# Kernel tuning notes

Measured on AMD Instinct MI355X. Metric: run time of the kernel, lower is better.

## Reference

```python
import jax, jax.numpy as jnp
import numpy as np

NV = 6890          # SMPL vertex count
NF = 13776         # SMPL face count
N_CHUNKS = 10
EUCL_THRES = 0.02  # euclthres
WN_THRES = 0.99    # exterior if winding number <= 0.99


def _winding_numbers(points, tris):
    """Generalized winding numbers of `points` [m,3] w.r.t. triangle soup `tris` [f,3,3].
    Solid angle per (point, triangle) via the van-Oosterom/Strackee atan2 formula."""
    r = tris[None, :, :, :] - points[:, None, None, :]   # [m,f,3,3]
    ra, rb, rc = r[:, :, 0, :], r[:, :, 1, :], r[:, :, 2, :]
    la = jnp.linalg.norm(ra, axis=-1)
    lb = jnp.linalg.norm(rb, axis=-1)
    lc = jnp.linalg.norm(rc, axis=-1)
    det = jnp.einsum('mfi,mfi->mf', ra, jnp.cross(rb, rc))
    denom = (la * lb * lc
             + jnp.sum(ra * rb, -1) * lc
             + jnp.sum(rb * rc, -1) * la
             + jnp.sum(rc * ra, -1) * lb)
    omega = 2.0 * jnp.arctan2(det, denom)                # [m,f]
    return jnp.sum(omega, axis=-1) / (4.0 * jnp.pi)      # [m]


def setup_inputs() -> dict:
    key = jax.random.key(0)
    k1, k2, k3 = jax.random.split(key, 3)
    vertices = jax.random.normal(k1, (1, NV, 3), dtype=jnp.float32)
    faces = jax.random.randint(k2, (NF, 3), 0, NV)
    # geodesic-distance >= geothres mask: symmetric, False on the diagonal
    gm = jax.random.uniform(k3, (NV, NV)) > 0.3
    gm = gm & gm.T
    gm = gm.at[jnp.arange(NV), jnp.arange(NV)].set(False)
    return {"vertices": vertices, "faces": faces, "geomask": gm}


def reference(vertices, faces, geomask):
    # triangles(vertices): gather face corner coordinates  [NF,3,3] (bs=1)
    tris = vertices[0][faces]
    # get_intersection_mask: chunked winding numbers, exterior = wn <= 0.99
    pts = vertices[0].reshape(N_CHUNKS, NV // N_CHUNKS, 3)
    wn = jax.lax.map(lambda p: _winding_numbers(p, tris), pts).reshape(NV)
    exterior = (wn <= WN_THRES)[None, :]                 # [1,NV] bool
    # batch_pairwise_dist (squared=False)
    x = vertices[0]                                      # [NV,3]
    sq = jnp.sum(x * x, axis=-1)
    d2 = sq[:, None] + sq[None, :] - 2.0 * (x @ x.T)
    v2v = jnp.sqrt(jnp.maximum(d2, 0.0))                 # [NV,NV]
    # mask geodesically-near pairs with inf, take per-vertex min over dim 1
    masked = jnp.where(geomask, v2v, jnp.inf)
    idx = jnp.argmin(masked, axis=0)                     # argmin over rows for each column
    v2v_min = v2v[jnp.arange(NV), idx][None, :]          # gather along dim 2 (symmetric)
    incontact = v2v_min < EUCL_THRES
    return v2v_min, incontact, exterior
```

## Files before the change

### kernel.cpp

```cpp
#include <hip/hip_runtime.h>
#include <math.h>

#define NV 6890
#define NF 13776
#define NVPAD 6912
#define NFPAD 13824
#define HALF 3456
#define PBLK 14
#define TCH 64
#define TPC 216
#define WN_BLOCKS (PBLK*TCH)
#define V2V_BLOCKS 1723
#define RED_BLOCKS 27
#define WN_THRES 0.99
#define EUCL_THRES 0.02f

#define WS_TRIS_OFF   64
#define WS_X4_OFF     (64 + NFPAD*48)
#define WS_PART_OFF   (WS_X4_OFF + NVPAD*16)

__global__ __launch_bounds__(256) void prep_kernel(
    const float* __restrict__ verts, const int* __restrict__ faces,
    const unsigned char* __restrict__ gm_bytes,
    float* __restrict__ tris12, float* __restrict__ x4, int* __restrict__ flag)
{
    int t = blockIdx.x * 256 + threadIdx.x;

    if (t < NFPAD) {
        float* o = tris12 + (size_t)t * 12;
        if (t < NF) {
            int ia = faces[t*3+0], ib = faces[t*3+1], ic = faces[t*3+2];
            o[0]  = verts[ia*3+0]; o[1]  = verts[ia*3+1]; o[2]  = verts[ia*3+2]; o[3]  = 0.f;
            o[4]  = verts[ib*3+0]; o[5]  = verts[ib*3+1]; o[6]  = verts[ib*3+2]; o[7]  = 0.f;
            o[8]  = verts[ic*3+0]; o[9]  = verts[ic*3+1]; o[10] = verts[ic*3+2]; o[11] = 0.f;
        } else {
            #pragma unroll
            for (int q = 0; q < 12; ++q) o[q] = 0.f;
        }
    }
    if (t < NVPAD) {
        if (t < NV) {
            float x = verts[t*3+0], y = verts[t*3+1], z = verts[t*3+2];
            x4[t*4+0] = x; x4[t*4+1] = y; x4[t*4+2] = z;
            x4[t*4+3] = (x*x + y*y) + z*z;
        } else {
            x4[t*4+0] = 0.f; x4[t*4+1] = 0.f; x4[t*4+2] = 0.f; x4[t*4+3] = 0.f;
        }
    }
    if (blockIdx.x == 0 && threadIdx.x < 64) {
        int lane = threadIdx.x;
        bool any3F = false, anyNZmod = false;
        for (int k = 0; k < 64; ++k) {
            int off = lane * 64 + k;
            unsigned char b = gm_bytes[off];
            if ((off & 3) == 3 && (b == 0x3F || b == 0xBF)) any3F = true;
            if ((off & 3) != 0 && b != 0) anyNZmod = true;
        }
        unsigned long long m3F = __ballot(any3F);
        unsigned long long mNZ = __ballot(anyNZmod);
        if (lane == 0) {
            *flag = m3F ? 2 : (mNZ ? 0 : 1);
        }
    }
}

__device__ __forceinline__ float fast_atan2f(float y, float x)
{
    float ay = __builtin_fabsf(y), ax = __builtin_fabsf(x);
    float mx = fmaxf(ax, ay);
    float mn = fminf(ax, ay);
    float r  = __builtin_amdgcn_rcpf(fmaxf(mx, 1e-37f));
    float t  = mn * r;
    float s  = t * t;
    float u  =              0.00282363896258175373077393f;
    u = fmaf(u, s, -0.0159569028764963150024414f);
    u = fmaf(u, s,  0.0425049886107444763183594f);
    u = fmaf(u, s, -0.0748900920152664184570312f);
    u = fmaf(u, s,  0.106347933411598205566406f);
    u = fmaf(u, s, -0.142027363181114196777344f);
    u = fmaf(u, s,  0.199926957488059997558594f);
    u = fmaf(u, s, -0.333331018686294555664062f);
    float p = fmaf(s * u, t, t);
    p = (ay > ax)  ? (1.5707963267948966f - p) : p;
    p = (x < 0.0f) ? (3.14159265358979323846f - p) : p;
    return copysignf(p, y);
}

#define TRI_OMEGA(A, B, C, PX, PY, PZ, S)                                 \
    {                                                                     \
        float ax = A.x - PX, ay = A.y - PY, az = A.z - PZ;                \
        float bx = B.x - PX, by = B.y - PY, bz = B.z - PZ;                \
        float cx = C.x - PX, cy = C.y - PY, cz = C.z - PZ;                \
        float la = __builtin_amdgcn_sqrtf((ax*ax + ay*ay) + az*az);       \
        float lb = __builtin_amdgcn_sqrtf((bx*bx + by*by) + bz*bz);       \
        float lc = __builtin_amdgcn_sqrtf((cx*cx + cy*cy) + cz*cz);       \
        float ux = by*cz - bz*cy;                                         \
        float uy = bz*cx - bx*cz;                                         \
        float uz = bx*cy - by*cx;                                         \
        float det = (ax*ux + ay*uy) + az*uz;                              \
        float dab = (ax*bx + ay*by) + az*bz;                              \
        float dbc = (bx*cx + by*cy) + bz*cz;                              \
        float dca = (cx*ax + cy*ay) + cz*az;                              \
        float denom = la*lb*lc + dab*lc + dbc*la + dca*lb;                \
        S += fast_atan2f(det, denom);                                     \
    }

__global__ __launch_bounds__(256) void fused_kernel(
    const float4* __restrict__ tris12, const float4* __restrict__ x4,
    float* __restrict__ partials,
    const void* __restrict__ gm, const int* __restrict__ flag_p,
    float* __restrict__ out)
{
    if (blockIdx.x < WN_BLOCKS) {
        int tc = blockIdx.x / PBLK;
        int pb = blockIdx.x - tc * PBLK;
        int pt = pb * 256 + threadIdx.x;
        if (pt >= HALF) return;
        int p1i = pt + HALF;

        float4 P0 = x4[pt];
        float4 P1 = x4[p1i];
        float px0 = P0.x, py0 = P0.y, pz0 = P0.z;
        float px1 = P1.x, py1 = P1.y, pz1 = P1.z;

        const float4* __restrict__ T = tris12 + (size_t)tc * (TPC * 3);

        float4 A0 = T[0], B0 = T[1], C0 = T[2];
        float4 A1 = T[3], B1 = T[4], C1 = T[5];
        double acc0 = 0.0, acc1 = 0.0;

        for (int kk = 0; kk < TPC; kk += 2) {
            int n0 = 3 * min(kk + 2, TPC - 1);
            int n1 = 3 * min(kk + 3, TPC - 1);
            float s0 = 0.f, s1 = 0.f;

            TRI_OMEGA(A0, B0, C0, px0, py0, pz0, s0);
            TRI_OMEGA(A0, B0, C0, px1, py1, pz1, s1);
            A0 = T[n0]; B0 = T[n0 + 1]; C0 = T[n0 + 2];

            TRI_OMEGA(A1, B1, C1, px0, py0, pz0, s0);
            TRI_OMEGA(A1, B1, C1, px1, py1, pz1, s1);
            A1 = T[n1]; B1 = T[n1 + 1]; C1 = T[n1 + 2];

            acc0 += (double)s0;
            acc1 += (double)s1;
        }

        partials[(size_t)tc * NVPAD + pt]  = (float)acc0;
        partials[(size_t)tc * NVPAD + p1i] = (float)acc1;
    } else {
        int bid = blockIdx.x - WN_BLOCKS;
        int w = threadIdx.x >> 6;
        int lane = threadIdx.x & 63;
        int j = bid * 4 + w;
        if (j >= NV) return;

        int flag = *flag_p;
        float4 vj = x4[j];
        float m = INFINITY;

#define V2V_BODY(GTEST)                                            \
        {                                                          \
            int i0 = 0;                                            \
            for (; i0 + 64 <= NV; i0 += 64) {                      \
                int i = i0 + lane;                                 \
                bool g = (GTEST);                                  \
                float4 vi = x4[i];                                 \
                float dot = (vi.x*vj.x + vi.y*vj.y) + vi.z*vj.z;   \
                float d2  = vi.w + vj.w - 2.0f*dot;                \
                m = fminf(m, g ? d2 : INFINITY);                   \
            }                                                      \
            int i = i0 + lane;                                     \
            if (i < NV) {                                          \
                bool g = (GTEST);                                  \
                float4 vi = x4[i];                                 \
                float dot = (vi.x*vj.x + vi.y*vj.y) + vi.z*vj.z;   \
                float d2  = vi.w + vj.w - 2.0f*dot;                \
                m = fminf(m, g ? d2 : INFINITY);                   \
            }                                                      \
        }

        if (flag == 0) {
            const unsigned char* row = (const unsigned char*)gm + (size_t)j * NV;
            V2V_BODY(row[i] != 0)
        } else if (flag == 1) {
            const int* row = (const int*)gm + (size_t)j * NV;
            V2V_BODY(row[i] != 0)
        } else {
            const float* row = (const float*)gm + (size_t)j * NV;
            V2V_BODY(row[i] != 0.0f)
        }
#undef V2V_BODY

        #pragma unroll
        for (int k = 32; k > 0; k >>= 1)
            m = fminf(m, __shfl_xor(m, k, 64));
        if (lane == 0) {
            float d = __builtin_amdgcn_sqrtf(fmaxf(m, 0.f));
            out[j] = d;
            out[NV + j] = (d < EUCL_THRES) ? 1.f : 0.f;
        }
    }
}

__global__ __launch_bounds__(256) void wn_reduce_kernel(
    const float* __restrict__ partials, float* __restrict__ out_exterior)
{
    int pt = blockIdx.x * 256 + threadIdx.x;
    if (pt >= NV) return;
    double s = 0.0;
    for (int t = 0; t < TCH; ++t) s += (double)partials[(size_t)t * NVPAD + pt];
    double wn = (2.0 * s) / 12.566370614359172953850573533118;
    out_exterior[pt] = (wn <= WN_THRES) ? 1.0f : 0.0f;
}

extern "C" void kernel_launch(void* const* d_in, const int* in_sizes, int n_in,
                              void* d_out, int out_size, void* d_ws, size_t ws_size,
                              hipStream_t stream)
{
    const float* verts = (const float*)d_in[0];
    const int*   faces = (const int*)d_in[1];
    const void*  gm    = d_in[2];
    float* out = (float*)d_out;
    char* ws = (char*)d_ws;

    int*   flag     = (int*)ws;
    float* tris12   = (float*)(ws + WS_TRIS_OFF);
    float* x4       = (float*)(ws + WS_X4_OFF);
    float* partials = (float*)(ws + WS_PART_OFF);

    prep_kernel<<<NFPAD / 256, 256, 0, stream>>>(
        verts, faces, (const unsigned char*)gm, tris12, x4, flag);

    fused_kernel<<<WN_BLOCKS + V2V_BLOCKS, 256, 0, stream>>>(
        (const float4*)tris12, (const float4*)x4, partials, gm, flag, out);

    wn_reduce_kernel<<<RED_BLOCKS, 256, 0, stream>>>(partials, out + 2 * NV);
}
```

Measured before the change: 441.4 us.

## Precompute all-pairs vertex distance table and reuse it for winding numbers and v2v

Adds a kernel that builds a dense NV×NVPAD table of vertex-to-vertex distances. The winding-number kernel then reads the corner distances from it and derives the dot products from per-face edge lengths, a normal and a plane offset computed in prep, so the per-pair sqrt and cross-product work goes away. The v2v min pass reads distances from the table instead of recomputing them. This trades ALU work for about 190MB of table writes and gathered reads whose row indices depend on the face, and it falls back to the old path when the workspace is too small.

```diff
diff --git a/kernel.cpp b/kernel.cpp
--- a/kernel.cpp
+++ b/kernel.cpp
@@ -6,33 +6,61 @@
 #define NVPAD 6912
 #define NFPAD 13824
 #define HALF 3456
-#define PBLK 14
-#define TCH 64
-#define TPC 216
-#define WN_BLOCKS (PBLK*TCH)
 #define V2V_BLOCKS 1723
 #define RED_BLOCKS 27
 #define WN_THRES 0.99
 #define EUCL_THRES 0.02f
 
+#define TCH_FB 64
+#define TPC_FB 216
+#define PBLK_FB 14
+#define WNB_FB (TCH_FB*PBLK_FB)
+#define TCH_TB 128
+#define TPC_TB 108
+#define PBLK_TB 14
+#define WNB_TB (TCH_TB*PBLK_TB)
+
 #define WS_TRIS_OFF   64
 #define WS_X4_OFF     (64 + NFPAD*48)
 #define WS_PART_OFF   (WS_X4_OFF + NVPAD*16)
+#define WS_TAB_OFF    (((WS_PART_OFF + TCH_TB*NVPAD*4) + 255) & ~(size_t)255)
+#define WS_TAB_BYTES  ((size_t)NV * NVPAD * 4)
 
 __global__ __launch_bounds__(256) void prep_kernel(
     const float* __restrict__ verts, const int* __restrict__ faces,
     const unsigned char* __restrict__ gm_bytes,
-    float* __restrict__ tris12, float* __restrict__ x4, int* __restrict__ flag)
+    float* __restrict__ tris, float* __restrict__ x4, int* __restrict__ flag,
+    int mode)
 {
     int t = blockIdx.x * 256 + threadIdx.x;
 
     if (t < NFPAD) {
-        float* o = tris12 + (size_t)t * 12;
+        float* o = tris + (size_t)t * 12;
         if (t < NF) {
             int ia = faces[t*3+0], ib = faces[t*3+1], ic = faces[t*3+2];
-            o[0]  = verts[ia*3+0]; o[1]  = verts[ia*3+1]; o[2]  = verts[ia*3+2]; o[3]  = 0.f;
-            o[4]  = verts[ib*3+0]; o[5]  = verts[ib*3+1]; o[6]  = verts[ib*3+2]; o[7]  = 0.f;
-            o[8]  = verts[ic*3+0]; o[9]  = verts[ic*3+1]; o[10] = verts[ic*3+2]; o[11] = 0.f;
+            float Ax = verts[ia*3+0], Ay = verts[ia*3+1], Az = verts[ia*3+2];
+            float Bx = verts[ib*3+0], By = verts[ib*3+1], Bz = verts[ib*3+2];
+            float Cx = verts[ic*3+0], Cy = verts[ic*3+1], Cz = verts[ic*3+2];
+            if (mode == 0) {
+                o[0]=Ax; o[1]=Ay; o[2]=Az;  o[3]=0.f;
+                o[4]=Bx; o[5]=By; o[6]=Bz;  o[7]=0.f;
+                o[8]=Cx; o[9]=Cy; o[10]=Cz; o[11]=0.f;
+            } else {
+                float e1x=Bx-Ax, e1y=By-Ay, e1z=Bz-Az;
+                float e2x=Cx-Ax, e2y=Cy-Ay, e2z=Cz-Az;
+                float nx = e1y*e2z - e1z*e2y;
+                float ny = e1z*e2x - e1x*e2z;
+                float nz = e1x*e2y - e1y*e2x;
+                float d0 = (nx*Ax + ny*Ay) + nz*Az;
+                float eab = (e1x*e1x + e1y*e1y) + e1z*e1z;
+                float bcx=Cx-Bx, bcy=Cy-By, bcz=Cz-Bz;
+                float ebc = (bcx*bcx + bcy*bcy) + bcz*bcz;
+                float eca = (e2x*e2x + e2y*e2y) + e2z*e2z;
+                o[0]=nx; o[1]=ny; o[2]=nz; o[3]=d0;
+                o[4]=eab; o[5]=ebc; o[6]=eca; o[7]=0.f;
+                o[8]=__int_as_float(ia); o[9]=__int_as_float(ib);
+                o[10]=__int_as_float(ic); o[11]=0.f;
+            }
         } else {
             #pragma unroll
             for (int q = 0; q < 12; ++q) o[q] = 0.f;
@@ -58,10 +86,19 @@
         }
         unsigned long long m3F = __ballot(any3F);
         unsigned long long mNZ = __ballot(anyNZmod);
-        if (lane == 0) {
-            *flag = m3F ? 2 : (mNZ ? 0 : 1);
-        }
-    }
+        if (lane == 0) *flag = m3F ? 2 : (mNZ ? 0 : 1);
+    }
+}
+
+__global__ __launch_bounds__(256) void tab_kernel(
+    const float4* __restrict__ x4, float* __restrict__ D)
+{
+    int p = blockIdx.x * 256 + threadIdx.x;
+    int v = blockIdx.y;
+    float4 Pv = x4[v];
+    float4 Pp = x4[p];
+    float dx = Pv.x - Pp.x, dy = Pv.y - Pp.y, dz = Pv.z - Pp.z;
+    D[(size_t)v * NVPAD + p] = __builtin_amdgcn_sqrtf((dx*dx + dy*dy) + dz*dz);
 }
 
 __device__ __forceinline__ float fast_atan2f(float y, float x)
@@ -86,6 +123,124 @@
     return copysignf(p, y);
 }
 
+#define OMEGA_TAB(LA, LB, LC, PX, PY, PZ, S)                               \
+    {                                                                      \
+        float la2 = LA*LA, lb2 = LB*LB, lc2 = LC*LC;                       \
+        float dab = (la2 + lb2 - eab) * 0.5f;                              \
+        float dbc = (lb2 + lc2 - ebc) * 0.5f;                              \
+        float dca = (lc2 + la2 - eca) * 0.5f;                              \
+        float det = d0 - ((nx*PX + ny*PY) + nz*PZ);                        \
+        float t3  = (LA*LB)*LC;                                            \
+        float denom = fmaf(dca, LB, fmaf(dbc, LA, fmaf(dab, LC, t3)));     \
+        float o = fast_atan2f(det, denom);                                 \
+        S += (t3 != 0.0f) ? o : 0.0f;   \
+    }
+
+__global__ __launch_bounds__(256) void fused_tab_kernel(
+    const float* __restrict__ consts, const float* __restrict__ Dt,
+    const float4* __restrict__ x4, float* __restrict__ partials,
+    const void* __restrict__ gm, const int* __restrict__ flag_p,
+    float* __restrict__ out)
+{
+    if (blockIdx.x < WNB_TB) {
+        int tc = blockIdx.x / PBLK_TB;
+        int pb = blockIdx.x - tc * PBLK_TB;
+        int pt = pb * 256 + threadIdx.x;
+        if (pt >= HALF) return;
+        int ptH = pt + HALF;
+
+        float4 P0 = x4[pt];
+        float4 P1 = x4[ptH];
+
+        const float* cvb = consts + (size_t)tc * TPC_TB * 12;
+        double acc0 = 0.0, acc1 = 0.0;
+
+        for (int k = 0; k < TPC_TB; k += 2) {
+            float s0 = 0.f, s1 = 0.f;
+            #pragma unroll
+            for (int u = 0; u < 2; ++u) {
+                const float* cv = cvb + (size_t)(k + u) * 12;
+                float nx = cv[0], ny = cv[1], nz = cv[2], d0 = cv[3];
+                float eab = cv[4], ebc = cv[5], eca = cv[6];
+                int ia = __float_as_int(cv[8]);
+                int ib = __float_as_int(cv[9]);
+                int ic = __float_as_int(cv[10]);
+                const float* rA = Dt + (size_t)ia * NVPAD;
+                const float* rB = Dt + (size_t)ib * NVPAD;
+                const float* rC = Dt + (size_t)ic * NVPAD;
+                float la0 = rA[pt],  lb0 = rB[pt],  lc0 = rC[pt];
+                float la1 = rA[ptH], lb1 = rB[ptH], lc1 = rC[ptH];
+                OMEGA_TAB(la0, lb0, lc0, P0.x, P0.y, P0.z, s0);
+                OMEGA_TAB(la1, lb1, lc1, P1.x, P1.y, P1.z, s1);
+            }
+            acc0 += (double)s0;
+            acc1 += (double)s1;
+        }
+
+        float* prow = partials + (size_t)tc * NVPAD;
+        prow[pt]  = (float)acc0;
+        prow[ptH] = (float)acc1;
+    } else {
+        int bid = blockIdx.x - WNB_TB;
+        int w = threadIdx.x >> 6;
+        int lane = threadIdx.x & 63;
+        int j = bid * 4 + w;
+        if (j >= NV) return;
+
+        int flag = *flag_p;
+        const float* Dr = Dt + (size_t)j * NVPAD;
+        float m = INFINITY;
+
+#define V2V_TAB(GTEST)                                             \
+        {                                                          \
+            int i0 = 0;                                            \
+            _Pragma("unroll 4")                                    \
+            for (; i0 + 64 <= NV; i0 += 64) {                      \
+                int i = i0 + lane;                                 \
+                bool g = (GTEST);                                  \
+                float d = Dr[i];                                   \
+                m = fminf(m, g ? d : INFINITY);                    \
+            }                                                      \
+            int i = i0 + lane;                                     \
+            if (i < NV) {                                          \
+                bool g = (GTEST);                                  \
+                float d = Dr[i];                                   \
+                m = fminf(m, g ? d : INFINITY);                    \
+            }                                                      \
+        }
+        if (flag == 0) {
+            const unsigned char* row = (const unsigned char*)gm + (size_t)j * NV;
+            V2V_TAB(row[i] != 0)
+        } else if (flag == 1) {
+            const int* row = (const int*)gm + (size_t)j * NV;
+            V2V_TAB(row[i] != 0)
+        } else {
+            const float* row = (const float*)gm + (size_t)j * NV;
+            V2V_TAB(row[i] != 0.0f)
+        }
+#undef V2V_TAB
+
+        #pragma unroll
+        for (int k = 32; k > 0; k >>= 1)
+            m = fminf(m, __shfl_xor(m, k, 64));
+        if (lane == 0) {
+            out[j] = m;
+            out[NV + j] = (m < EUCL_THRES) ? 1.f : 0.f;
+        }
+    }
+}
+
+__global__ __launch_bounds__(256) void reduce_tab_kernel(
+    const float* __restrict__ partials, float* __restrict__ out_exterior)
+{
+    int pt = blockIdx.x * 256 + threadIdx.x;
+    if (pt >= NV) return;
+    double s = 0.0;
+    for (int t = 0; t < TCH_TB; ++t) s += (double)partials[(size_t)t * NVPAD + pt];
+    double wn = (2.0 * s) / 12.566370614359172953850573533118;
+    out_exterior[pt] = (wn <= WN_THRES) ? 1.0f : 0.0f;
+}
+
 #define TRI_OMEGA(A, B, C, PX, PY, PZ, S)                                 \
     {                                                                     \
         float ax = A.x - PX, ay = A.y - PY, az = A.z - PZ;                \
@@ -105,15 +260,15 @@
         S += fast_atan2f(det, denom);                                     \
     }
 
-__global__ __launch_bounds__(256) void fused_kernel(
+__global__ __launch_bounds__(256) void fused_fb_kernel(
     const float4* __restrict__ tris12, const float4* __restrict__ x4,
     float* __restrict__ partials,
     const void* __restrict__ gm, const int* __restrict__ flag_p,
     float* __restrict__ out)
 {
-    if (blockIdx.x < WN_BLOCKS) {
-        int tc = blockIdx.x / PBLK;
-        int pb = blockIdx.x - tc * PBLK;
+    if (blockIdx.x < WNB_FB) {
+        int tc = blockIdx.x / PBLK_FB;
+        int pb = blockIdx.x - tc * PBLK_FB;
         int pt = pb * 256 + threadIdx.x;
         if (pt >= HALF) return;
         int p1i = pt + HALF;
@@ -123,15 +278,15 @@
         float px0 = P0.x, py0 = P0.y, pz0 = P0.z;
         float px1 = P1.x, py1 = P1.y, pz1 = P1.z;
 
-        const float4* __restrict__ T = tris12 + (size_t)tc * (TPC * 3);
+        const float4* __restrict__ T = tris12 + (size_t)tc * (TPC_FB * 3);
 
         float4 A0 = T[0], B0 = T[1], C0 = T[2];
         float4 A1 = T[3], B1 = T[4], C1 = T[5];
         double acc0 = 0.0, acc1 = 0.0;
 
-        for (int kk = 0; kk < TPC; kk += 2) {
-            int n0 = 3 * min(kk + 2, TPC - 1);
-            int n1 = 3 * min(kk + 3, TPC - 1);
+        for (int kk = 0; kk < TPC_FB; kk += 2) {
+            int n0 = 3 * min(kk + 2, TPC_FB - 1);
+            int n1 = 3 * min(kk + 3, TPC_FB - 1);
             float s0 = 0.f, s1 = 0.f;
 
             TRI_OMEGA(A0, B0, C0, px0, py0, pz0, s0);
@@ -149,7 +304,7 @@
         partials[(size_t)tc * NVPAD + pt]  = (float)acc0;
         partials[(size_t)tc * NVPAD + p1i] = (float)acc1;
     } else {
-        int bid = blockIdx.x - WN_BLOCKS;
+        int bid = blockIdx.x - WNB_FB;
         int w = threadIdx.x >> 6;
         int lane = threadIdx.x & 63;
         int j = bid * 4 + w;
@@ -162,6 +317,7 @@
 #define V2V_BODY(GTEST)                                            \
         {                                                          \
             int i0 = 0;                                            \
+            _Pragma("unroll 4")                                    \
             for (; i0 + 64 <= NV; i0 += 64) {                      \
                 int i = i0 + lane;                                 \
                 bool g = (GTEST);                                  \
@@ -179,7 +335,6 @@
                 m = fminf(m, g ? d2 : INFINITY);                   \
             }                                                      \
         }
-
         if (flag == 0) {
             const unsigned char* row = (const unsigned char*)gm + (size_t)j * NV;
             V2V_BODY(row[i] != 0)
@@ -203,13 +358,13 @@
     }
 }
 
-__global__ __launch_bounds__(256) void wn_reduce_kernel(
+__global__ __launch_bounds__(256) void reduce_fb_kernel(
     const float* __restrict__ partials, float* __restrict__ out_exterior)
 {
     int pt = blockIdx.x * 256 + threadIdx.x;
     if (pt >= NV) return;
     double s = 0.0;
-    for (int t = 0; t < TCH; ++t) s += (double)partials[(size_t)t * NVPAD + pt];
+    for (int t = 0; t < TCH_FB; ++t) s += (double)partials[(size_t)t * NVPAD + pt];
     double wn = (2.0 * s) / 12.566370614359172953850573533118;
     out_exterior[pt] = (wn <= WN_THRES) ? 1.0f : 0.0f;
 }
@@ -225,15 +380,25 @@
     char* ws = (char*)d_ws;
 
     int*   flag     = (int*)ws;
-    float* tris12   = (float*)(ws + WS_TRIS_OFF);
+    float* tris     = (float*)(ws + WS_TRIS_OFF);
     float* x4       = (float*)(ws + WS_X4_OFF);
     float* partials = (float*)(ws + WS_PART_OFF);
-
-    prep_kernel<<<NFPAD / 256, 256, 0, stream>>>(
-        verts, faces, (const unsigned char*)gm, tris12, x4, flag);
-
-    fused_kernel<<<WN_BLOCKS + V2V_BLOCKS, 256, 0, stream>>>(
-        (const float4*)tris12, (const float4*)x4, partials, gm, flag, out);
-
-    wn_reduce_kernel<<<RED_BLOCKS, 256, 0, stream>>>(partials, out + 2 * NV);
-}
+    float* Dt       = (float*)(ws + WS_TAB_OFF);
+
+    size_t need = (size_t)WS_TAB_OFF + WS_TAB_BYTES;
+    if (ws_size >= need) {
+        prep_kernel<<<NFPAD / 256, 256, 0, stream>>>(
+            verts, faces, (const unsigned char*)gm, tris, x4, flag, 1);
+        tab_kernel<<<dim3(NVPAD / 256, NV), 256, 0, stream>>>(
+            (const float4*)x4, Dt);
+        fused_tab_kernel<<<WNB_TB + V2V_BLOCKS, 256, 0, stream>>>(
+            tris, Dt, (const float4*)x4, partials, gm, flag, out);
+        reduce_tab_kernel<<<RED_BLOCKS, 256, 0, stream>>>(partials, out + 2 * NV);
+    } else {
+        prep_kernel<<<NFPAD / 256, 256, 0, stream>>>(
+            verts, faces, (const unsigned char*)gm, tris, x4, flag, 0);
+        fused_fb_kernel<<<WNB_FB + V2V_BLOCKS, 256, 0, stream>>>(
+            (const float4*)tris, (const float4*)x4, partials, gm, flag, out);
+        reduce_fb_kernel<<<RED_BLOCKS, 256, 0, stream>>>(partials, out + 2 * NV);
+    }
+}
```

Measured after the change: 454.1 us. 1.03x slower.
